# Performance work log

Hardware: AMD Instinct MI355X
Metric: run time of the kernel (lower is better)

The kernel has to match this reference:

```python
import jax, jax.numpy as jnp
import numpy as np

# Model dims (match init_kwargs)
D, L = 64, 262144          # data_size
G, J = 8, 8                # number of relations, dims per relation
FG = 16                    # filters (kernel_size) per relation
W = 31                     # window_size
PAD1 = (W - 1) // 2        # 15, left padding in the original code
F = G * FG                 # 128 total filters


def setup_inputs() -> dict:
    key = jax.random.key(0)
    k1, k2 = jax.random.split(key)
    x = jax.random.normal(k1, (D, L), dtype=jnp.float32)
    # original uses torch.rand for Parameter init -> uniform [0,1)
    params = jax.random.uniform(k2, (G, FG, J, W), dtype=jnp.float32)
    # dim_relation = [[0..7],[8..15],...,[56..63]] == arange reshaped
    rel_idx = jnp.arange(G * J, dtype=jnp.int32).reshape(G, J)
    return {"x": x, "params": params, "rel_idx": rel_idx}


def _forward(x, params, rel_idx):
    xg = x[rel_idx]                                   # [G, J, L] gather relation dims

    # Interior positions (PAD1 <= k <= L-W+PAD1): full-window correlation.
    # Expressed as a grouped 1D conv (lax conv is cross-correlation, matching
    # the original data*kernel elementwise-sum, no kernel flip).
    lhs = xg.reshape(1, G * J, L)                     # [N=1, C=G*J, L]
    rhs = params.reshape(G * FG, J, W)                # [O=G*FG, I=J, W]
    y = jax.lax.conv_general_dilated(
        lhs, rhs, window_strides=(1,),
        padding=[(PAD1, W - 1 - PAD1)],
        dimension_numbers=("NCH", "OIH", "NCH"),
        feature_group_count=G,
    )[0].reshape(G, FG, L)

    # Left boundary (k < PAD1): the original aligns kernel[0] with x[...,0]
    # and truncates BOTH at k+W-PAD1, i.e. y[k] = sum_{w < k+W-PAD1} xg[:, :, w]*K[..., w]
    # (NOT zero padding). Cumulative sum over w gives all prefixes at once.
    pl = jnp.einsum("gjw,gfjw->gfw", xg[:, :, :W], params)      # [G, FG, W]
    left_c = jnp.cumsum(pl, axis=-1)
    y = y.at[:, :, :PAD1].set(left_c[:, :, W - PAD1 - 1: W - 1])

    # Right boundary (k > L-W+PAD1): kernel[-1] aligned with x[..., L-1],
    # truncated at the front: y[k] = sum_{w >= W-m} xg[:, :, L-W+w]*K[..., w],
    # with m = L-k+PAD1. Reverse cumsum gives all suffixes.
    pr = jnp.einsum("gjw,gfjw->gfw", xg[:, :, L - W:], params)  # [G, FG, W]
    right_c = jnp.cumsum(pr[:, :, ::-1], axis=-1)[:, :, ::-1]    # suffix sums
    n_right = W - 1 - PAD1                                       # positions k = L-W+PAD1+1 .. L-1
    y = y.at[:, :, L - n_right:].set(right_c[:, :, 1: W - PAD1])

    return y.reshape(F * L, 1)                        # matches y.view(-1, 1)


def reference(x, params, rel_idx):
    return _forward(x, params, rel_idx)
```

## Files before the change

### kernel.cpp

```cpp
#include <hip/hip_runtime.h>

#define LL    262144
#define GG    8
#define JJ    8
#define FGF   16
#define WW    31
#define PAD1  15
#define NB    2048
#define NTHR  512
#define XTLEN (NB + 32)

typedef __bf16 bf16x8 __attribute__((ext_vector_type(8)));
typedef float  f32x4  __attribute__((ext_vector_type(4)));

__device__ inline unsigned short f2bf(float f) {
    unsigned int u = __float_as_uint(f);
    u = (u + 0x7FFF + ((u >> 16) & 1)) >> 16;
    return (unsigned short)u;
}

__global__ __launch_bounds__(NTHR, 6)
void conv_mfma(const float* __restrict__ x, const float* __restrict__ p,
               const int* __restrict__ rel, float* __restrict__ out)
{
    __shared__ unsigned short pw[32 * 16 * 8];
    __shared__ unsigned short xt[XTLEN * 8];

    const int t = threadIdx.x;
    const int g = blockIdx.y;
    const long nbase = (long)blockIdx.x * NB;

    const long r0 = rel[g * JJ + 0], r1 = rel[g * JJ + 1];
    const long r2 = rel[g * JJ + 2], r3 = rel[g * JJ + 3];
    const long r4 = rel[g * JJ + 4], r5 = rel[g * JJ + 5];
    const long r6 = rel[g * JJ + 6], r7 = rel[g * JJ + 7];

    {
        #pragma unroll
        for (int it = 0; it < (XTLEN + NTHR - 1) / NTHR; ++it) {
            int c = t + it * NTHR;
            if (c < XTLEN) {
                long gp = nbase - 16 + c;
                unsigned int w0, w1, w2, w3;
                if (gp >= 0 && gp < LL) {
                    float v0 = x[r0 * LL + gp], v1 = x[r1 * LL + gp];
                    float v2 = x[r2 * LL + gp], v3 = x[r3 * LL + gp];
                    float v4 = x[r4 * LL + gp], v5 = x[r5 * LL + gp];
                    float v6 = x[r6 * LL + gp], v7 = x[r7 * LL + gp];
                    w0 = (unsigned int)f2bf(v0) | ((unsigned int)f2bf(v1) << 16);
                    w1 = (unsigned int)f2bf(v2) | ((unsigned int)f2bf(v3) << 16);
                    w2 = (unsigned int)f2bf(v4) | ((unsigned int)f2bf(v5) << 16);
                    w3 = (unsigned int)f2bf(v6) | ((unsigned int)f2bf(v7) << 16);
                } else {
                    w0 = w1 = w2 = w3 = 0u;
                }
                uint4 pk; pk.x = w0; pk.y = w1; pk.z = w2; pk.w = w3;
                *(uint4*)&xt[c * 8] = pk;
            }
        }
    }

    {
        const float* pg = p + (long)g * FGF * JJ * WW;
        #pragma unroll
        for (int k = 0; k < 8; ++k) {
            int i = t + k * NTHR;
            int w = i >> 7;
            int f = (i >> 3) & 15;
            int j = i & 7;
            float v = (w < WW) ? pg[(f * JJ + j) * WW + w] : 0.0f;
            pw[i] = f2bf(v);
        }
    }
    __syncthreads();

    const int lane = t & 63;
    const int wid  = t >> 6;
    const int col  = lane & 15;
    const int q    = lane >> 4;

    bf16x8 b[8];
    #pragma unroll
    for (int s = 0; s < 8; ++s)
        b[s] = *(const bf16x8*)&pw[((s * 4 + q) * 16 + col) * 8];

    const int pb = wid * 256 + col + q + 1;

    #define LDX(pos) (*(const bf16x8*)&xt[(pos) * 8])

    bf16x8 F0a = LDX(pb + 0), F0b = LDX(pb + 4), F0c = LDX(pb + 8), F0d = LDX(pb + 12);

    #pragma unroll
    for (int T = 0; T < 16; ++T) {
        const int o = pb + T * 16 + 16;
        bf16x8 F1a = LDX(o + 0), F1b = LDX(o + 4), F1c = LDX(o + 8), F1d = LDX(o + 12);

        f32x4 acc = {0.f, 0.f, 0.f, 0.f};
        acc = __builtin_amdgcn_mfma_f32_16x16x32_bf16(F0a, b[0], acc, 0, 0, 0);
        acc = __builtin_amdgcn_mfma_f32_16x16x32_bf16(F0b, b[1], acc, 0, 0, 0);
        acc = __builtin_amdgcn_mfma_f32_16x16x32_bf16(F0c, b[2], acc, 0, 0, 0);
        acc = __builtin_amdgcn_mfma_f32_16x16x32_bf16(F0d, b[3], acc, 0, 0, 0);
        acc = __builtin_amdgcn_mfma_f32_16x16x32_bf16(F1a, b[4], acc, 0, 0, 0);
        acc = __builtin_amdgcn_mfma_f32_16x16x32_bf16(F1b, b[5], acc, 0, 0, 0);
        acc = __builtin_amdgcn_mfma_f32_16x16x32_bf16(F1c, b[6], acc, 0, 0, 0);
        acc = __builtin_amdgcn_mfma_f32_16x16x32_bf16(F1d, b[7], acc, 0, 0, 0);

        const long kc0 = nbase + (long)(wid * 256 + T * 16) + q * 4;
        const size_t ro = (size_t)(g * FGF + col) * LL;
        *(f32x4*)&out[ro + kc0] = acc;

        F0a = F1a; F0b = F1b; F0c = F1c; F0d = F1d;
    }
    #undef LDX

    if (blockIdx.x == 0 || blockIdx.x == (LL / NB - 1)) {
        __syncthreads();
        if (t < 256) {
            const int f  = t >> 4;
            const int qq = t & 15;
            if (qq < PAD1) {
                const bool left = (blockIdx.x == 0);
                float a = 0.0f;
                for (int j = 0; j < JJ; ++j) {
                    const float* pf = p + (((long)(g * FGF + f)) * JJ + j) * WW;
                    const float* xj = x + (long)rel[g * JJ + j] * LL + (left ? 0 : LL - WW);
                    #pragma unroll
                    for (int w = 0; w < WW; ++w) {
                        bool use = left ? (w <= qq + PAD1) : (w >= qq + 1);
                        if (use) a += xj[w] * pf[w];
                    }
                }
                const size_t ro = (size_t)(g * FGF + f) * LL;
                out[ro + (left ? (long)qq : (long)(LL - PAD1) + qq)] = a;
            }
        }
    }
}

extern "C" void kernel_launch(void* const* d_in, const int* in_sizes, int n_in,
                              void* d_out, int out_size, void* d_ws, size_t ws_size,
                              hipStream_t stream)
{
    const float* x   = (const float*)d_in[0];
    const float* p   = (const float*)d_in[1];
    const int*   rel = (const int*)d_in[2];
    float* out = (float*)d_out;

    dim3 grid(LL / NB, GG);
    conv_mfma<<<grid, NTHR, 0, stream>>>(x, p, rel, out);
}
```

Before: 215.8 us.

## Split into transpose-to-bf16 prepass and LDS-free MFMA conv kernel using workspace

Adds a prepass kernel that reads x with float4 loads, converts it to bf16 and writes an interleaved, zero-padded [G][L+32][8] layout into workspace, and also pre-packs the bf16 weights. A second kernel then loads MFMA operands straight from global memory, with no shared-memory staging or barrier, using smaller 512-position blocks. The aim is to replace the original scattered scalar loads and LDS staging with coalesced vector accesses and to raise occupancy. The cost is an extra launch plus a round trip of about 32 MB of bf16 data through workspace. If the workspace is too small, the old fused kernel is used instead.

Result: slower. 250.2 us (+15.9%).

```diff
diff --git a/kernel.cpp b/kernel.cpp
--- a/kernel.cpp
+++ b/kernel.cpp
@@ -6,9 +6,7 @@
 #define FGF   16
 #define WW    31
 #define PAD1  15
-#define NB    2048
-#define NTHR  512
-#define XTLEN (NB + 32)
+#define LPAD  (LL + 32)
 
 typedef __bf16 bf16x8 __attribute__((ext_vector_type(8)));
 typedef float  f32x4  __attribute__((ext_vector_type(4)));
@@ -19,80 +17,92 @@
     return (unsigned short)u;
 }
 
-__global__ __launch_bounds__(NTHR, 6)
-void conv_mfma(const float* __restrict__ x, const float* __restrict__ p,
-               const int* __restrict__ rel, float* __restrict__ out)
-{
-    __shared__ unsigned short pw[32 * 16 * 8];
-    __shared__ unsigned short xt[XTLEN * 8];
-
+__global__ __launch_bounds__(256)
+void k_xpose(const float* __restrict__ x, const float* __restrict__ p,
+             const int* __restrict__ rel, unsigned short* __restrict__ xw,
+             unsigned short* __restrict__ pwg)
+{
     const int t = threadIdx.x;
     const int g = blockIdx.y;
-    const long nbase = (long)blockIdx.x * NB;
+    const long gp0 = (long)blockIdx.x * 1024 + t * 4;
 
     const long r0 = rel[g * JJ + 0], r1 = rel[g * JJ + 1];
     const long r2 = rel[g * JJ + 2], r3 = rel[g * JJ + 3];
     const long r4 = rel[g * JJ + 4], r5 = rel[g * JJ + 5];
     const long r6 = rel[g * JJ + 6], r7 = rel[g * JJ + 7];
 
-    {
-        #pragma unroll
-        for (int it = 0; it < (XTLEN + NTHR - 1) / NTHR; ++it) {
-            int c = t + it * NTHR;
-            if (c < XTLEN) {
-                long gp = nbase - 16 + c;
-                unsigned int w0, w1, w2, w3;
-                if (gp >= 0 && gp < LL) {
-                    float v0 = x[r0 * LL + gp], v1 = x[r1 * LL + gp];
-                    float v2 = x[r2 * LL + gp], v3 = x[r3 * LL + gp];
-                    float v4 = x[r4 * LL + gp], v5 = x[r5 * LL + gp];
-                    float v6 = x[r6 * LL + gp], v7 = x[r7 * LL + gp];
-                    w0 = (unsigned int)f2bf(v0) | ((unsigned int)f2bf(v1) << 16);
-                    w1 = (unsigned int)f2bf(v2) | ((unsigned int)f2bf(v3) << 16);
-                    w2 = (unsigned int)f2bf(v4) | ((unsigned int)f2bf(v5) << 16);
-                    w3 = (unsigned int)f2bf(v6) | ((unsigned int)f2bf(v7) << 16);
-                } else {
-                    w0 = w1 = w2 = w3 = 0u;
-                }
-                uint4 pk; pk.x = w0; pk.y = w1; pk.z = w2; pk.w = w3;
-                *(uint4*)&xt[c * 8] = pk;
-            }
-        }
-    }
-
-    {
+    float4 v0 = *(const float4*)&x[r0 * LL + gp0];
+    float4 v1 = *(const float4*)&x[r1 * LL + gp0];
+    float4 v2 = *(const float4*)&x[r2 * LL + gp0];
+    float4 v3 = *(const float4*)&x[r3 * LL + gp0];
+    float4 v4 = *(const float4*)&x[r4 * LL + gp0];
+    float4 v5 = *(const float4*)&x[r5 * LL + gp0];
+    float4 v6 = *(const float4*)&x[r6 * LL + gp0];
+    float4 v7 = *(const float4*)&x[r7 * LL + gp0];
+
+    const size_t base = (size_t)g * LPAD + gp0 + 16;
+    #define PACKC(C, off)                                                     \
+        {   uint4 pk;                                                         \
+            pk.x = (unsigned)f2bf(v0.C) | ((unsigned)f2bf(v1.C) << 16);       \
+            pk.y = (unsigned)f2bf(v2.C) | ((unsigned)f2bf(v3.C) << 16);       \
+            pk.z = (unsigned)f2bf(v4.C) | ((unsigned)f2bf(v5.C) << 16);       \
+            pk.w = (unsigned)f2bf(v6.C) | ((unsigned)f2bf(v7.C) << 16);       \
+            *(uint4*)&xw[(base + (off)) * 8] = pk; }
+    PACKC(x, 0) PACKC(y, 1) PACKC(z, 2) PACKC(w, 3)
+    #undef PACKC
+
+    if (blockIdx.x == 0 && t < 32) {
+        size_t idx = (size_t)g * LPAD + ((t < 16) ? (size_t)t
+                                                  : (size_t)LL + t);
+        uint4 z = {0u, 0u, 0u, 0u};
+        *(uint4*)&xw[idx * 8] = z;
+    }
+
+    if (blockIdx.x == 1) {
         const float* pg = p + (long)g * FGF * JJ * WW;
         #pragma unroll
-        for (int k = 0; k < 8; ++k) {
-            int i = t + k * NTHR;
+        for (int k = 0; k < 16; ++k) {
+            int i = t + k * 256;
             int w = i >> 7;
             int f = (i >> 3) & 15;
             int j = i & 7;
             float v = (w < WW) ? pg[(f * JJ + j) * WW + w] : 0.0f;
-            pw[i] = f2bf(v);
-        }
-    }
-    __syncthreads();
+            pwg[g * 4096 + i] = f2bf(v);
+        }
+    }
+}
+
+__global__ __launch_bounds__(256, 4)
+void k_conv(const unsigned short* __restrict__ xw,
+            const unsigned short* __restrict__ pwg,
+            const float* __restrict__ x, const float* __restrict__ p,
+            const int* __restrict__ rel, float* __restrict__ out)
+{
+    const int t = threadIdx.x;
+    const int g = blockIdx.y;
+    const long nbase = (long)blockIdx.x * 512;
 
     const int lane = t & 63;
     const int wid  = t >> 6;
     const int col  = lane & 15;
     const int q    = lane >> 4;
 
+    const unsigned short* xg = xw + (size_t)g * LPAD * 8;
+    const unsigned short* pg = pwg + g * 4096;
+
     bf16x8 b[8];
     #pragma unroll
     for (int s = 0; s < 8; ++s)
-        b[s] = *(const bf16x8*)&pw[((s * 4 + q) * 16 + col) * 8];
-
-    const int pb = wid * 256 + col + q + 1;
-
-    #define LDX(pos) (*(const bf16x8*)&xt[(pos) * 8])
+        b[s] = *(const bf16x8*)&pg[((s * 4 + q) * 16 + col) * 8];
+
+    const long pb = nbase + wid * 128 + col + q + 1;
+    #define LDX(pp) (*(const bf16x8*)&xg[(pp) * 8])
 
     bf16x8 F0a = LDX(pb + 0), F0b = LDX(pb + 4), F0c = LDX(pb + 8), F0d = LDX(pb + 12);
 
     #pragma unroll
-    for (int T = 0; T < 16; ++T) {
-        const int o = pb + T * 16 + 16;
+    for (int T = 0; T < 8; ++T) {
+        const long o = pb + T * 16 + 16;
         bf16x8 F1a = LDX(o + 0), F1b = LDX(o + 4), F1c = LDX(o + 8), F1d = LDX(o + 12);
 
         f32x4 acc = {0.f, 0.f, 0.f, 0.f};
@@ -105,19 +115,120 @@
         acc = __builtin_amdgcn_mfma_f32_16x16x32_bf16(F1c, b[6], acc, 0, 0, 0);
         acc = __builtin_amdgcn_mfma_f32_16x16x32_bf16(F1d, b[7], acc, 0, 0, 0);
 
+        const long kc0 = nbase + (long)(wid * 128 + T * 16) + q * 4;
+        const size_t ro = (size_t)(g * FGF + col) * LL;
+        *(f32x4*)&out[ro + kc0] = acc;
+
+        F0a = F1a; F0b = F1b; F0c = F1c; F0d = F1d;
+    }
+    #undef LDX
+
+    if (blockIdx.x == 0 || blockIdx.x == (LL / 512 - 1)) {
+        __syncthreads();
+        const int f  = t >> 4;
+        const int qq = t & 15;
+        if (qq < PAD1) {
+            const bool left = (blockIdx.x == 0);
+            float a = 0.0f;
+            for (int j = 0; j < JJ; ++j) {
+                const float* pf = p + (((long)(g * FGF + f)) * JJ + j) * WW;
+                const float* xj = x + (long)rel[g * JJ + j] * LL + (left ? 0 : LL - WW);
+                #pragma unroll
+                for (int w = 0; w < WW; ++w) {
+                    bool use = left ? (w <= qq + PAD1) : (w >= qq + 1);
+                    if (use) a += xj[w] * pf[w];
+                }
+            }
+            const size_t ro = (size_t)(g * FGF + f) * LL;
+            out[ro + (left ? (long)qq : (long)(LL - PAD1) + qq)] = a;
+        }
+    }
+}
+
+#define NBF   2048
+#define NTHF  512
+#define XTLEN (NBF + 32)
+__global__ __launch_bounds__(NTHF, 6)
+void conv_fused(const float* __restrict__ x, const float* __restrict__ p,
+                const int* __restrict__ rel, float* __restrict__ out)
+{
+    __shared__ unsigned short pw[32 * 16 * 8];
+    __shared__ unsigned short xt[XTLEN * 8];
+
+    const int t = threadIdx.x;
+    const int g = blockIdx.y;
+    const long nbase = (long)blockIdx.x * NBF;
+
+    const long r0 = rel[g * JJ + 0], r1 = rel[g * JJ + 1];
+    const long r2 = rel[g * JJ + 2], r3 = rel[g * JJ + 3];
+    const long r4 = rel[g * JJ + 4], r5 = rel[g * JJ + 5];
+    const long r6 = rel[g * JJ + 6], r7 = rel[g * JJ + 7];
+
+    #pragma unroll
+    for (int it = 0; it < (XTLEN + NTHF - 1) / NTHF; ++it) {
+        int c = t + it * NTHF;
+        if (c < XTLEN) {
+            long gp = nbase - 16 + c;
+            unsigned int w0, w1, w2, w3;
+            if (gp >= 0 && gp < LL) {
+                float v0 = x[r0 * LL + gp], v1 = x[r1 * LL + gp];
+                float v2 = x[r2 * LL + gp], v3 = x[r3 * LL + gp];
+                float v4 = x[r4 * LL + gp], v5 = x[r5 * LL + gp];
+                float v6 = x[r6 * LL + gp], v7 = x[r7 * LL + gp];
+                w0 = (unsigned)f2bf(v0) | ((unsigned)f2bf(v1) << 16);
+                w1 = (unsigned)f2bf(v2) | ((unsigned)f2bf(v3) << 16);
+                w2 = (unsigned)f2bf(v4) | ((unsigned)f2bf(v5) << 16);
+                w3 = (unsigned)f2bf(v6) | ((unsigned)f2bf(v7) << 16);
+            } else { w0 = w1 = w2 = w3 = 0u; }
+            uint4 pk; pk.x = w0; pk.y = w1; pk.z = w2; pk.w = w3;
+            *(uint4*)&xt[c * 8] = pk;
+        }
+    }
+    {
+        const float* pgq = p + (long)g * FGF * JJ * WW;
+        #pragma unroll
+        for (int k = 0; k < 8; ++k) {
+            int i = t + k * NTHF;
+            int w = i >> 7, f = (i >> 3) & 15, j = i & 7;
+            float v = (w < WW) ? pgq[(f * JJ + j) * WW + w] : 0.0f;
+            pw[i] = f2bf(v);
+        }
+    }
+    __syncthreads();
+
+    const int lane = t & 63, wid = t >> 6, col = lane & 15, q = lane >> 4;
+    bf16x8 b[8];
+    #pragma unroll
+    for (int s = 0; s < 8; ++s)
+        b[s] = *(const bf16x8*)&pw[((s * 4 + q) * 16 + col) * 8];
+
+    const int pb = wid * 256 + col + q + 1;
+    #define LDF(pos) (*(const bf16x8*)&xt[(pos) * 8])
+    bf16x8 F0a = LDF(pb + 0), F0b = LDF(pb + 4), F0c = LDF(pb + 8), F0d = LDF(pb + 12);
+    #pragma unroll
+    for (int T = 0; T < 16; ++T) {
+        const int o = pb + T * 16 + 16;
+        bf16x8 F1a = LDF(o + 0), F1b = LDF(o + 4), F1c = LDF(o + 8), F1d = LDF(o + 12);
+        f32x4 acc = {0.f, 0.f, 0.f, 0.f};
+        acc = __builtin_amdgcn_mfma_f32_16x16x32_bf16(F0a, b[0], acc, 0, 0, 0);
+        acc = __builtin_amdgcn_mfma_f32_16x16x32_bf16(F0b, b[1], acc, 0, 0, 0);
+        acc = __builtin_amdgcn_mfma_f32_16x16x32_bf16(F0c, b[2], acc, 0, 0, 0);
+        acc = __builtin_amdgcn_mfma_f32_16x16x32_bf16(F0d, b[3], acc, 0, 0, 0);
+        acc = __builtin_amdgcn_mfma_f32_16x16x32_bf16(F1a, b[4], acc, 0, 0, 0);
+        acc = __builtin_amdgcn_mfma_f32_16x16x32_bf16(F1b, b[5], acc, 0, 0, 0);
+        acc = __builtin_amdgcn_mfma_f32_16x16x32_bf16(F1c, b[6], acc, 0, 0, 0);
+        acc = __builtin_amdgcn_mfma_f32_16x16x32_bf16(F1d, b[7], acc, 0, 0, 0);
         const long kc0 = nbase + (long)(wid * 256 + T * 16) + q * 4;
         const size_t ro = (size_t)(g * FGF + col) * LL;
         *(f32x4*)&out[ro + kc0] = acc;
-
         F0a = F1a; F0b = F1b; F0c = F1c; F0d = F1d;
     }
-    #undef LDX
-
-    if (blockIdx.x == 0 || blockIdx.x == (LL / NB - 1)) {
+    #undef LDF
+
+    if (blockIdx.x == 0 || blockIdx.x == (LL / NBF - 1)) {
         __syncthreads();
         if (t < 256) {
-            const int f  = t >> 4;
-            const int qq = t & 15;
+            const int f = t >> 4, qq = t & 15;
             if (qq < PAD1) {
                 const bool left = (blockIdx.x == 0);
                 float a = 0.0f;
@@ -146,6 +257,15 @@
     const int*   rel = (const int*)d_in[2];
     float* out = (float*)d_out;
 
-    dim3 grid(LL / NB, GG);
-    conv_mfma<<<grid, NTHR, 0, stream>>>(x, p, rel, out);
-}
+    const size_t PWG_BYTES = (size_t)GG * 4096 * 2;
+    const size_t XW_BYTES  = (size_t)GG * LPAD * 8 * 2;
+
+    if (d_ws && ws_size >= PWG_BYTES + XW_BYTES) {
+        unsigned short* pwg = (unsigned short*)d_ws;
+        unsigned short* xw  = (unsigned short*)((char*)d_ws + PWG_BYTES);
+        k_xpose<<<dim3(LL / 1024, GG), 256, 0, stream>>>(x, p, rel, xw, pwg);
+        k_conv <<<dim3(LL / 512,  GG), 256, 0, stream>>>(xw, pwg, x, p, rel, out);
+    } else {
+        conv_fused<<<dim3(LL / NBF, GG), NTHF, 0, stream>>>(x, p, rel, out);
+    }
+}
```

## Stage x per wave in private LDS slices, removing block-wide barrier before compute

Applied to the files above, without the earlier changes.

Each wave now loads, converts and stores its own 288-slot window of x into a private LDS slice and processes two 256-position chunks sequentially. This drops the block-wide barrier between x staging and MFMA work, so one wave's global loads can overlap other waves' compute. The block shrinks to 256 threads with the span unchanged at 2048 positions, and the halo per chunk is reloaded, adding some redundant global reads and conversions. Weight staging now costs each thread 16 loads instead of 8.

Measured after the change: 232.2 us. 7.6% more time.

```diff
diff --git a/kernel.cpp b/kernel.cpp
--- a/kernel.cpp
+++ b/kernel.cpp
@@ -6,9 +6,13 @@
 #define FGF   16
 #define WW    31
 #define PAD1  15
-#define NB    2048
-#define NTHR  512
-#define XTLEN (NB + 32)
+#define CHUNK 256
+#define CPW   2
+#define WAVES 4
+#define NTHR  (WAVES * 64)
+#define SPAN  (WAVES * CPW * CHUNK)
+#define NBX   (LL / SPAN)
+#define SLOTS 288
 
 typedef __bf16 bf16x8 __attribute__((ext_vector_type(8)));
 typedef float  f32x4  __attribute__((ext_vector_type(4)));
@@ -19,16 +23,15 @@
     return (unsigned short)u;
 }
 
-__global__ __launch_bounds__(NTHR, 6)
+__global__ __launch_bounds__(NTHR, 4)
 void conv_mfma(const float* __restrict__ x, const float* __restrict__ p,
                const int* __restrict__ rel, float* __restrict__ out)
 {
     __shared__ unsigned short pw[32 * 16 * 8];
-    __shared__ unsigned short xt[XTLEN * 8];
+    __shared__ unsigned short xs[WAVES][SLOTS * 8];
 
     const int t = threadIdx.x;
     const int g = blockIdx.y;
-    const long nbase = (long)blockIdx.x * NB;
 
     const long r0 = rel[g * JJ + 0], r1 = rel[g * JJ + 1];
     const long r2 = rel[g * JJ + 2], r3 = rel[g * JJ + 3];
@@ -36,34 +39,9 @@
     const long r6 = rel[g * JJ + 6], r7 = rel[g * JJ + 7];
 
     {
-        #pragma unroll
-        for (int it = 0; it < (XTLEN + NTHR - 1) / NTHR; ++it) {
-            int c = t + it * NTHR;
-            if (c < XTLEN) {
-                long gp = nbase - 16 + c;
-                unsigned int w0, w1, w2, w3;
-                if (gp >= 0 && gp < LL) {
-                    float v0 = x[r0 * LL + gp], v1 = x[r1 * LL + gp];
-                    float v2 = x[r2 * LL + gp], v3 = x[r3 * LL + gp];
-                    float v4 = x[r4 * LL + gp], v5 = x[r5 * LL + gp];
-                    float v6 = x[r6 * LL + gp], v7 = x[r7 * LL + gp];
-                    w0 = (unsigned int)f2bf(v0) | ((unsigned int)f2bf(v1) << 16);
-                    w1 = (unsigned int)f2bf(v2) | ((unsigned int)f2bf(v3) << 16);
-                    w2 = (unsigned int)f2bf(v4) | ((unsigned int)f2bf(v5) << 16);
-                    w3 = (unsigned int)f2bf(v6) | ((unsigned int)f2bf(v7) << 16);
-                } else {
-                    w0 = w1 = w2 = w3 = 0u;
-                }
-                uint4 pk; pk.x = w0; pk.y = w1; pk.z = w2; pk.w = w3;
-                *(uint4*)&xt[c * 8] = pk;
-            }
-        }
-    }
-
-    {
         const float* pg = p + (long)g * FGF * JJ * WW;
         #pragma unroll
-        for (int k = 0; k < 8; ++k) {
+        for (int k = 0; k < 16; ++k) {
             int i = t + k * NTHR;
             int w = i >> 7;
             int f = (i >> 3) & 15;
@@ -84,55 +62,81 @@
     for (int s = 0; s < 8; ++s)
         b[s] = *(const bf16x8*)&pw[((s * 4 + q) * 16 + col) * 8];
 
-    const int pb = wid * 256 + col + q + 1;
-
-    #define LDX(pos) (*(const bf16x8*)&xt[(pos) * 8])
-
-    bf16x8 F0a = LDX(pb + 0), F0b = LDX(pb + 4), F0c = LDX(pb + 8), F0d = LDX(pb + 12);
+    unsigned short* xsl = &xs[wid][0];
+    const int pb = col + q + 1;
+    #define LDS8(pos) (*(const bf16x8*)&xsl[(pos) * 8])
 
     #pragma unroll
-    for (int T = 0; T < 16; ++T) {
-        const int o = pb + T * 16 + 16;
-        bf16x8 F1a = LDX(o + 0), F1b = LDX(o + 4), F1c = LDX(o + 8), F1d = LDX(o + 12);
+    for (int c = 0; c < CPW; ++c) {
+        const long W0 = (long)blockIdx.x * SPAN + (wid * CPW + c) * CHUNK;
 
-        f32x4 acc = {0.f, 0.f, 0.f, 0.f};
-        acc = __builtin_amdgcn_mfma_f32_16x16x32_bf16(F0a, b[0], acc, 0, 0, 0);
-        acc = __builtin_amdgcn_mfma_f32_16x16x32_bf16(F0b, b[1], acc, 0, 0, 0);
-        acc = __builtin_amdgcn_mfma_f32_16x16x32_bf16(F0c, b[2], acc, 0, 0, 0);
-        acc = __builtin_amdgcn_mfma_f32_16x16x32_bf16(F0d, b[3], acc, 0, 0, 0);
-        acc = __builtin_amdgcn_mfma_f32_16x16x32_bf16(F1a, b[4], acc, 0, 0, 0);
-        acc = __builtin_amdgcn_mfma_f32_16x16x32_bf16(F1b, b[5], acc, 0, 0, 0);
-        acc = __builtin_amdgcn_mfma_f32_16x16x32_bf16(F1c, b[6], acc, 0, 0, 0);
-        acc = __builtin_amdgcn_mfma_f32_16x16x32_bf16(F1d, b[7], acc, 0, 0, 0);
+        #pragma unroll
+        for (int pn = 0; pn < 5; ++pn) {
+            int pp = pn * 64 + lane;
+            if (pp < SLOTS) {
+                long gp = W0 - 16 + pp;
+                uint4 pk;
+                if (gp >= 0 && gp < LL) {
+                    float v0 = x[r0 * LL + gp], v1 = x[r1 * LL + gp];
+                    float v2 = x[r2 * LL + gp], v3 = x[r3 * LL + gp];
+                    float v4 = x[r4 * LL + gp], v5 = x[r5 * LL + gp];
+                    float v6 = x[r6 * LL + gp], v7 = x[r7 * LL + gp];
+                    pk.x = (unsigned)f2bf(v0) | ((unsigned)f2bf(v1) << 16);
+                    pk.y = (unsigned)f2bf(v2) | ((unsigned)f2bf(v3) << 16);
+                    pk.z = (unsigned)f2bf(v4) | ((unsigned)f2bf(v5) << 16);
+                    pk.w = (unsigned)f2bf(v6) | ((unsigned)f2bf(v7) << 16);
+                } else {
+                    pk.x = pk.y = pk.z = pk.w = 0u;
+                }
+                *(uint4*)&xsl[pp * 8] = pk;
+            }
+        }
 
-        const long kc0 = nbase + (long)(wid * 256 + T * 16) + q * 4;
-        const size_t ro = (size_t)(g * FGF + col) * LL;
-        *(f32x4*)&out[ro + kc0] = acc;
+        bf16x8 F0a = LDS8(pb + 0), F0b = LDS8(pb + 4),
+               F0c = LDS8(pb + 8), F0d = LDS8(pb + 12);
+        #pragma unroll
+        for (int T = 0; T < 16; ++T) {
+            const int o = pb + T * 16 + 16;
+            bf16x8 F1a = LDS8(o + 0), F1b = LDS8(o + 4),
+                   F1c = LDS8(o + 8), F1d = LDS8(o + 12);
 
-        F0a = F1a; F0b = F1b; F0c = F1c; F0d = F1d;
+            f32x4 acc = {0.f, 0.f, 0.f, 0.f};
+            acc = __builtin_amdgcn_mfma_f32_16x16x32_bf16(F0a, b[0], acc, 0, 0, 0);
+            acc = __builtin_amdgcn_mfma_f32_16x16x32_bf16(F0b, b[1], acc, 0, 0, 0);
+            acc = __builtin_amdgcn_mfma_f32_16x16x32_bf16(F0c, b[2], acc, 0, 0, 0);
+            acc = __builtin_amdgcn_mfma_f32_16x16x32_bf16(F0d, b[3], acc, 0, 0, 0);
+            acc = __builtin_amdgcn_mfma_f32_16x16x32_bf16(F1a, b[4], acc, 0, 0, 0);
+            acc = __builtin_amdgcn_mfma_f32_16x16x32_bf16(F1b, b[5], acc, 0, 0, 0);
+            acc = __builtin_amdgcn_mfma_f32_16x16x32_bf16(F1c, b[6], acc, 0, 0, 0);
+            acc = __builtin_amdgcn_mfma_f32_16x16x32_bf16(F1d, b[7], acc, 0, 0, 0);
+
+            const long kc0 = W0 + (long)T * 16 + q * 4;
+            const size_t ro = (size_t)(g * FGF + col) * LL;
+            *(f32x4*)&out[ro + kc0] = acc;
+
+            F0a = F1a; F0b = F1b; F0c = F1c; F0d = F1d;
+        }
     }
-    #undef LDX
+    #undef LDS8
 
-    if (blockIdx.x == 0 || blockIdx.x == (LL / NB - 1)) {
+    if (blockIdx.x == 0 || blockIdx.x == NBX - 1) {
         __syncthreads();
-        if (t < 256) {
-            const int f  = t >> 4;
-            const int qq = t & 15;
-            if (qq < PAD1) {
-                const bool left = (blockIdx.x == 0);
-                float a = 0.0f;
-                for (int j = 0; j < JJ; ++j) {
-                    const float* pf = p + (((long)(g * FGF + f)) * JJ + j) * WW;
-                    const float* xj = x + (long)rel[g * JJ + j] * LL + (left ? 0 : LL - WW);
-                    #pragma unroll
-                    for (int w = 0; w < WW; ++w) {
-                        bool use = left ? (w <= qq + PAD1) : (w >= qq + 1);
-                        if (use) a += xj[w] * pf[w];
-                    }
+        const int f  = t >> 4;
+        const int qq = t & 15;
+        if (qq < PAD1) {
+            const bool left = (blockIdx.x == 0);
+            float a = 0.0f;
+            for (int j = 0; j < JJ; ++j) {
+                const float* pf = p + (((long)(g * FGF + f)) * JJ + j) * WW;
+                const float* xj = x + (long)rel[g * JJ + j] * LL + (left ? 0 : LL - WW);
+                #pragma unroll
+                for (int w = 0; w < WW; ++w) {
+                    bool use = left ? (w <= qq + PAD1) : (w >= qq + 1);
+                    if (use) a += xj[w] * pf[w];
                 }
-                const size_t ro = (size_t)(g * FGF + f) * LL;
-                out[ro + (left ? (long)qq : (long)(LL - PAD1) + qq)] = a;
             }
+            const size_t ro = (size_t)(g * FGF + f) * LL;
+            out[ro + (left ? (long)qq : (long)(LL - PAD1) + qq)] = a;
         }
     }
 }
@@ -146,6 +150,6 @@
     const int*   rel = (const int*)d_in[2];
     float* out = (float*)d_out;
 
-    dim3 grid(LL / NB, GG);
+    dim3 grid(NBX, GG);
     conv_mfma<<<grid, NTHR, 0, stream>>>(x, p, rel, out);
 }
```
